# Performance work log

Hardware: AMD Instinct MI355X
Metric: run time of the kernel (lower is better)

The kernel has to match this reference:

```python
import jax, jax.numpy as jnp
import numpy as np

THRESH = 1.0
NBITS = 3
QMAX = float(2 ** NBITS - 1)
BN_EPS = 1e-5

T, B, IN_DIM = 500, 64, 440
HID, NLAYERS, OUT = 1024, 4, 1944


def fsq(v):
    # FakeSpikeQuantization (eval): quantize membrane potential to multiples of
    # threshold, clipped to [0, 2^n_bits - 1] levels; straight-through estimator.
    q = jnp.clip(jnp.round(v / THRESH), 0.0, QMAX) * THRESH
    return v + jax.lax.stop_gradient(q - v)


def input_fsq_scan(xs):
    # vmem += x; out = fsq(vmem); vmem -= out  -- sequential over time
    def step(vmem, x):
        vmem = vmem + x
        o = fsq(vmem)
        return vmem - o, o
    _, outs = jax.lax.scan(step, jnp.zeros_like(xs[0]), xs)
    return outs


def lif_scan(ws, tau):
    # syn = w_t + tau*prev_syn; vmem += syn; out = fsq(vmem); vmem -= out
    Bb, H = ws.shape[1], ws.shape[2]
    def step(carry, w_t):
        prev_syn, vmem = carry
        syn = w_t + tau * prev_syn
        vmem = vmem + syn
        o = fsq(vmem)
        return (syn, vmem - o), o
    init = (jnp.zeros((Bb, H), ws.dtype), jnp.zeros((Bb, H), ws.dtype))
    _, outs = jax.lax.scan(step, init, ws)
    return outs


def bn_eval(x, gamma, beta):
    # BatchNorm1d in eval mode with default running stats (mean=0, var=1)
    return x / jnp.sqrt(1.0 + BN_EPS) * gamma + beta


def setup_inputs() -> dict:
    key = jax.random.key(0)
    ks = jax.random.split(key, 10)
    xs = jax.random.normal(ks[0], (T, B, IN_DIM), dtype=jnp.float32)
    # kaiming-uniform-like init scales
    W0 = jax.random.uniform(ks[1], (HID, IN_DIM), minval=-1.0, maxval=1.0) * np.sqrt(1.0 / IN_DIM)
    Ws = jax.random.uniform(ks[2], (NLAYERS - 1, HID, HID), minval=-1.0, maxval=1.0) * np.sqrt(1.0 / HID)
    taus = jnp.ones((NLAYERS, HID), dtype=jnp.float32)
    bn_gamma = jnp.ones((NLAYERS, HID), dtype=jnp.float32)
    bn_beta = jnp.zeros((NLAYERS, HID), dtype=jnp.float32)
    bound = np.sqrt(0.01 / (HID + OUT))
    Wf = jax.random.uniform(ks[3], (OUT, HID), minval=-bound, maxval=bound).astype(jnp.float32)
    fbn_gamma = jnp.ones((OUT,), dtype=jnp.float32)
    fbn_beta = jnp.zeros((OUT,), dtype=jnp.float32)
    return {"xs": xs, "W0": W0, "Ws": Ws, "taus": taus, "bn_gamma": bn_gamma,
            "bn_beta": bn_beta, "Wf": Wf, "fbn_gamma": fbn_gamma, "fbn_beta": fbn_beta}


def reference(xs, W0, Ws, taus, bn_gamma, bn_beta, Wf, fbn_gamma, fbn_beta):
    # input spike quantization
    inps = input_fsq_scan(xs)  # [T,B,IN]
    n_layers = taus.shape[0]
    for l in range(n_layers):
        W = W0 if l == 0 else Ws[l - 1]
        ws = jnp.einsum('tbi,hi->tbh', inps, W)          # dense projection (no bias; use_bn)
        ws = bn_eval(ws, bn_gamma[l], bn_beta[l])
        inps = lif_scan(ws, taus[l])                     # [T,B,H]
    logits = jnp.einsum('tbh,oh->tbo', inps, Wf)         # final linear (no bias)
    logits = bn_eval(logits, fbn_gamma, fbn_beta)
    Tt, Bb, O = logits.shape
    return jax.nn.log_softmax(logits.reshape(Tt * Bb, O), axis=1)
```

## Files before the change

### kernel.cpp

```cpp
#include <hip/hip_runtime.h>
#include <hip/hip_bf16.h>
#include <cstddef>

typedef signed char i8;
typedef unsigned int u32;
typedef int intx4 __attribute__((ext_vector_type(4)));
typedef float floatx4 __attribute__((ext_vector_type(4)));

#define T_STEPS 500
#define BATCH 64
#define INDIM 440
#define INPAD 512
#define HID 1024
#define OUTDIM 1944
#define OUTPAD 2048
#define MROWS 32000
#define INV_SQRT_BN 0.9999950000374997f
#define CH 20

__device__ __forceinline__ void g2lds16(const void* g, void* l) {
  __builtin_amdgcn_global_load_lds(
      (const __attribute__((address_space(1))) u32*)g,
      (__attribute__((address_space(3))) u32*)l, 16, 0, 0);
}

__global__ __launch_bounds__(256) void input_fsq_k(const float* __restrict__ xs,
                                                   i8* __restrict__ sp0) {
  int tid = blockIdx.x * 256 + threadIdx.x;
  int b = tid >> 9;
  int i = tid & 511;
  bool act = (i < INDIM);
  const float* src = xs + (size_t)b * INDIM + (act ? i : (INDIM - 1));
  i8* dst = sp0 + (size_t)b * INPAD + i;
  float fact = act ? 1.f : 0.f;
  const int LS = BATCH * INDIM;
  const int SS = BATCH * INPAD;
  float vmem = 0.f;
  float bufA[CH], bufB[CH];
#pragma unroll
  for (int j = 0; j < CH; ++j) bufA[j] = src[(size_t)j * LS];
  for (int it = 0; it < 12; ++it) {
    const int t0 = it * 2 * CH;
#pragma unroll
    for (int j = 0; j < CH; ++j) bufB[j] = src[(size_t)(t0 + CH + j) * LS];
#pragma unroll
    for (int j = 0; j < CH; ++j) {
      vmem += bufA[j] * fact;
      float q = fminf(fmaxf(rintf(vmem), 0.f), 7.f);
      vmem -= q;
      dst[(size_t)(t0 + j) * SS] = (i8)q;
    }
#pragma unroll
    for (int j = 0; j < CH; ++j) bufA[j] = src[(size_t)(t0 + 2 * CH + j) * LS];
#pragma unroll
    for (int j = 0; j < CH; ++j) {
      vmem += bufB[j] * fact;
      float q = fminf(fmaxf(rintf(vmem), 0.f), 7.f);
      vmem -= q;
      dst[(size_t)(t0 + CH + j) * SS] = (i8)q;
    }
  }
  const int t0 = 24 * CH;
#pragma unroll
  for (int j = 0; j < CH; ++j) {
    vmem += bufA[j] * fact;
    float q = fminf(fmaxf(rintf(vmem), 0.f), 7.f);
    vmem -= q;
    dst[(size_t)(t0 + j) * SS] = (i8)q;
  }
}

__global__ __launch_bounds__(256) void lif_k(const float* __restrict__ ws,
                                             const float* __restrict__ taus,
                                             i8* __restrict__ sp) {
  int tid = blockIdx.x * 256 + threadIdx.x;
  float tau = taus[tid & (HID - 1)];
  const float* src = ws + tid;
  i8* dst = sp + tid;
  const int S = BATCH * HID;
  float syn = 0.f, vmem = 0.f;
  float bufA[CH], bufB[CH];
#pragma unroll
  for (int j = 0; j < CH; ++j) bufA[j] = src[(size_t)j * S];
  for (int it = 0; it < 12; ++it) {
    const int t0 = it * 2 * CH;
#pragma unroll
    for (int j = 0; j < CH; ++j) bufB[j] = src[(size_t)(t0 + CH + j) * S];
#pragma unroll
    for (int j = 0; j < CH; ++j) {
      syn = fmaf(tau, syn, bufA[j]);
      vmem += syn;
      float q = fminf(fmaxf(rintf(vmem), 0.f), 7.f);
      vmem -= q;
      dst[(size_t)(t0 + j) * S] = (i8)q;
    }
#pragma unroll
    for (int j = 0; j < CH; ++j) bufA[j] = src[(size_t)(t0 + 2 * CH + j) * S];
#pragma unroll
    for (int j = 0; j < CH; ++j) {
      syn = fmaf(tau, syn, bufB[j]);
      vmem += syn;
      float q = fminf(fmaxf(rintf(vmem), 0.f), 7.f);
      vmem -= q;
      dst[(size_t)(t0 + CH + j) * S] = (i8)q;
    }
  }
  const int t0 = 24 * CH;
#pragma unroll
  for (int j = 0; j < CH; ++j) {
    syn = fmaf(tau, syn, bufA[j]);
    vmem += syn;
    float q = fminf(fmaxf(rintf(vmem), 0.f), 7.f);
    vmem -= q;
    dst[(size_t)(t0 + j) * S] = (i8)q;
  }
}

__global__ __launch_bounds__(256) void quant_rows_k(
    const float* __restrict__ W, const float* __restrict__ g,
    i8* __restrict__ Q1, i8* __restrict__ Q2,
    float* __restrict__ S1, float* __restrict__ S2,
    int K_in, int K_out, int nvalid) {
  int row = blockIdx.x * 4 + (threadIdx.x >> 6);
  int lane = threadIdx.x & 63;
  bool valid = row < nvalid;
  float gm = valid ? g[row] * INV_SQRT_BN : 0.f;
  const float* src = W + (size_t)row * K_in;
  float w[16], r[16];
  const int ne = K_out >> 6;
  float mx = 0.f;
  for (int e = 0; e < ne; ++e) {
    int k = lane + (e << 6);
    float v = (valid && k < K_in) ? src[k] * gm : 0.f;
    w[e] = v;
    mx = fmaxf(mx, fabsf(v));
  }
#pragma unroll
  for (int o = 32; o; o >>= 1) mx = fmaxf(mx, __shfl_xor(mx, o));
  float s1 = (mx > 0.f) ? mx * (1.f / 127.f) : 1.f;
  float inv1 = 1.f / s1;
  float mr = 0.f;
  for (int e = 0; e < ne; ++e) {
    float q = fminf(fmaxf(rintf(w[e] * inv1), -127.f), 127.f);
    Q1[(size_t)row * K_out + lane + (e << 6)] = (i8)q;
    float res = fmaf(-s1, q, w[e]);
    r[e] = res;
    mr = fmaxf(mr, fabsf(res));
  }
#pragma unroll
  for (int o = 32; o; o >>= 1) mr = fmaxf(mr, __shfl_xor(mr, o));
  float s2 = (mr > 0.f) ? mr * (1.f / 127.f) : 1.f;
  float inv2 = 1.f / s2;
  for (int e = 0; e < ne; ++e) {
    float q = fminf(fmaxf(rintf(r[e] * inv2), -127.f), 127.f);
    Q2[(size_t)row * K_out + lane + (e << 6)] = (i8)q;
  }
  if (lane == 0) {
    S1[row] = s1;
    S2[row] = s2;
  }
}

template <int DUAL>
__global__ __launch_bounds__(256, 2) void gemm_i8(
    const i8* __restrict__ A, const i8* __restrict__ B1q,
    const i8* __restrict__ B2q, const float* __restrict__ S1,
    const float* __restrict__ S2, const float* __restrict__ bias,
    float* __restrict__ C, int K, int ldc, int ncols) {
  extern __shared__ char smem[];
  char* As = smem;
  char* Bs1 = As + 128 * 128;
  char* Bs2 = DUAL ? Bs1 + 128 * 128 : Bs1;

  const int tid = threadIdx.x;
  const int m0 = blockIdx.y * 128;
  const int n0 = blockIdx.x * 128;
  const int lane = tid & 63;
  const int wave = tid >> 6;
  const int wm = (wave & 1) * 64;
  const int wn = (wave >> 1) * 64;
  const int lr = lane & 15;
  const int lq = lane >> 4;

  intx4 acc1[4][4], acc2[DUAL ? 4 : 1][4];
#pragma unroll
  for (int i = 0; i < 4; ++i)
#pragma unroll
    for (int j = 0; j < 4; ++j) {
      intx4 z = {0, 0, 0, 0};
      acc1[i][j] = z;
      if (DUAL) acc2[i][j] = z;
    }

  const int srow = tid >> 3;
  const int sj = (tid & 7) ^ (srow & 7);
  const i8* ga = A + (size_t)(m0 + srow) * K + sj * 16;
  const i8* gb1 = B1q + (size_t)(n0 + srow) * K + sj * 16;
  const i8* gb2 = DUAL ? B2q + (size_t)(n0 + srow) * K + sj * 16 : (const i8*)nullptr;
  const int ldso = tid * 16;
  const int sw = lr & 7;

  for (int k0 = 0; k0 < K; k0 += 128) {
#pragma unroll
    for (int it = 0; it < 4; ++it) {
      g2lds16(ga + (size_t)(it * 32) * K + k0, As + ldso + it * 4096);
      g2lds16(gb1 + (size_t)(it * 32) * K + k0, Bs1 + ldso + it * 4096);
      if (DUAL) g2lds16(gb2 + (size_t)(it * 32) * K + k0, Bs2 + ldso + it * 4096);
    }
    __syncthreads();
#pragma unroll
    for (int kk = 0; kk < 2; ++kk) {
      const int jc = kk * 4 + lq;
      const int co = ((jc ^ sw) << 4);
      intx4 af[4];
#pragma unroll
      for (int i = 0; i < 4; ++i)
        af[i] = *(const intx4*)(As + (wm + i * 16 + lr) * 128 + co);
#pragma unroll
      for (int j = 0; j < 4; ++j) {
        const int bo = (wn + j * 16 + lr) * 128 + co;
        intx4 b1 = *(const intx4*)(Bs1 + bo);
#pragma unroll
        for (int i = 0; i < 4; ++i)
          acc1[i][j] = __builtin_amdgcn_mfma_i32_16x16x64_i8(af[i], b1, acc1[i][j], 0, 0, 0);
        if (DUAL) {
          intx4 b2 = *(const intx4*)(Bs2 + bo);
#pragma unroll
          for (int i = 0; i < 4; ++i)
            acc2[i][j] = __builtin_amdgcn_mfma_i32_16x16x64_i8(af[i], b2, acc2[i][j], 0, 0, 0);
        }
      }
    }
    __syncthreads();
  }

  float* Es = (float*)smem;
  const int rq = lq * 4;
  const int rbase = (wave & 1) * 16;
  float s1v[4], s2v[4], bv[4];
#pragma unroll
  for (int j = 0; j < 4; ++j) {
    int cg = n0 + wn + j * 16 + lr;
    s1v[j] = S1[cg];
    s2v[j] = DUAL ? S2[cg] : 0.f;
    bv[j] = (cg < ncols) ? bias[cg] : 0.f;
  }
#pragma unroll
  for (int i = 0; i < 4; ++i) {
    __syncthreads();
#pragma unroll
    for (int j = 0; j < 4; ++j) {
      int cl = wn + j * 16 + lr;
#pragma unroll
      for (int r = 0; r < 4; ++r) {
        float v = fmaf(s1v[j], (float)acc1[i][j][r], bv[j]);
        if (DUAL) v = fmaf(s2v[j], (float)acc2[i][j][r], v);
        Es[(rbase + rq + r) * 132 + cl] = v;
      }
    }
    __syncthreads();
#pragma unroll
    for (int ps = 0; ps < 4; ++ps) {
      int rl = ps * 8 + (tid >> 5);
      int c4 = (tid & 31) * 4;
      floatx4 v = *(const floatx4*)(Es + rl * 132 + c4);
      int rg = m0 + (rl >> 4) * 64 + i * 16 + (rl & 15);
      int cg = n0 + c4;
      if (cg < ncols)
        *(floatx4*)(C + (size_t)rg * ldc + cg) = v;
    }
  }
}

__global__ __launch_bounds__(256) void logsoftmax_k(float* __restrict__ data) {
  __shared__ float red[8];
  float* p = data + (size_t)blockIdx.x * OUTDIM;
  const int t = threadIdx.x;
  float v[8];
  float mx = -1e30f;
#pragma unroll
  for (int j = 0; j < 8; ++j) {
    int c = t + j * 256;
    v[j] = (c < OUTDIM) ? p[c] : -1e30f;
    mx = fmaxf(mx, v[j]);
  }
#pragma unroll
  for (int o = 32; o > 0; o >>= 1) mx = fmaxf(mx, __shfl_down(mx, o));
  if ((t & 63) == 0) red[t >> 6] = mx;
  __syncthreads();
  mx = fmaxf(fmaxf(red[0], red[1]), fmaxf(red[2], red[3]));
  float s = 0.f;
#pragma unroll
  for (int j = 0; j < 8; ++j) {
    int c = t + j * 256;
    if (c < OUTDIM) s += __expf(v[j] - mx);
  }
#pragma unroll
  for (int o = 32; o > 0; o >>= 1) s += __shfl_down(s, o);
  if ((t & 63) == 0) red[4 + (t >> 6)] = s;
  __syncthreads();
  s = (red[4] + red[5]) + (red[6] + red[7]);
  float lse = mx + __logf(s);
#pragma unroll
  for (int j = 0; j < 8; ++j) {
    int c = t + j * 256;
    if (c < OUTDIM) p[c] = v[j] - lse;
  }
}

extern "C" void kernel_launch(void* const* d_in, const int* in_sizes, int n_in,
                              void* d_out, int out_size, void* d_ws, size_t ws_size,
                              hipStream_t stream) {
  const float* xs = (const float*)d_in[0];
  const float* W0 = (const float*)d_in[1];
  const float* Ws = (const float*)d_in[2];
  const float* taus = (const float*)d_in[3];
  const float* bng = (const float*)d_in[4];
  const float* bnb = (const float*)d_in[5];
  const float* Wf = (const float*)d_in[6];
  const float* fg = (const float*)d_in[7];
  const float* fb = (const float*)d_in[8];
  float* out = (float*)d_out;

  char* p = (char*)d_ws;
  i8* sp0 = (i8*)p;    p += (size_t)MROWS * INPAD;
  i8* sp = (i8*)p;     p += (size_t)MROWS * HID;
  float* wsb = (float*)p; p += (size_t)MROWS * HID * 4;
  i8* Q1_0 = (i8*)p;   p += (size_t)HID * INPAD;
  i8* Q2_0 = (i8*)p;   p += (size_t)HID * INPAD;
  i8* Q1_l = (i8*)p;   p += (size_t)3 * HID * HID;
  i8* Q2_l = (i8*)p;   p += (size_t)3 * HID * HID;
  i8* Q1_f = (i8*)p;   p += (size_t)OUTPAD * HID;
  i8* Q2_f = (i8*)p;   p += (size_t)OUTPAD * HID;
  float* S1_0 = (float*)p; p += HID * 4;
  float* S2_0 = (float*)p; p += HID * 4;
  float* S1_l = (float*)p; p += 3 * HID * 4;
  float* S2_l = (float*)p; p += 3 * HID * 4;
  float* S1_f = (float*)p; p += OUTPAD * 4;
  float* S2_f = (float*)p; p += OUTPAD * 4;

  input_fsq_k<<<(BATCH * INPAD) / 256, 256, 0, stream>>>(xs, sp0);
  quant_rows_k<<<HID / 4, 256, 0, stream>>>(W0, bng, Q1_0, Q2_0, S1_0, S2_0,
                                            INDIM, INPAD, HID);
  for (int l = 1; l < 4; ++l)
    quant_rows_k<<<HID / 4, 256, 0, stream>>>(
        Ws + (size_t)(l - 1) * HID * HID, bng + l * HID,
        Q1_l + (size_t)(l - 1) * HID * HID, Q2_l + (size_t)(l - 1) * HID * HID,
        S1_l + (l - 1) * HID, S2_l + (l - 1) * HID, HID, HID, HID);
  quant_rows_k<<<OUTPAD / 4, 256, 0, stream>>>(Wf, fg, Q1_f, Q2_f, S1_f, S2_f,
                                               HID, HID, OUTDIM);

  gemm_i8<1><<<dim3(HID / 128, MROWS / 128), 256, 48 * 1024, stream>>>(
      sp0, Q1_0, Q2_0, S1_0, S2_0, bnb, wsb, INPAD, HID, HID);
  lif_k<<<(BATCH * HID) / 256, 256, 0, stream>>>(wsb, taus, sp);
  for (int l = 1; l < 4; ++l) {
    gemm_i8<1><<<dim3(HID / 128, MROWS / 128), 256, 48 * 1024, stream>>>(
        sp, Q1_l + (size_t)(l - 1) * HID * HID, Q2_l + (size_t)(l - 1) * HID * HID,
        S1_l + (l - 1) * HID, S2_l + (l - 1) * HID, bnb + l * HID, wsb,
        HID, HID, HID);
    lif_k<<<(BATCH * HID) / 256, 256, 0, stream>>>(wsb, taus + l * HID, sp);
  }
  gemm_i8<0><<<dim3(OUTPAD / 128, MROWS / 128), 256, 32 * 1024, stream>>>(
      sp, Q1_f, (const i8*)nullptr, S1_f, (const float*)nullptr, fb, out,
      HID, OUTDIM, OUTDIM);
  logsoftmax_k<<<MROWS, 256, 0, stream>>>(out);
}
```

Before: 893.4 us.

## Double-buffer A tile in LDS and stream B fragments directly from global

```diff
diff --git a/kernel.cpp b/kernel.cpp
--- a/kernel.cpp
+++ b/kernel.cpp
@@ -166,96 +166,136 @@
     const i8* __restrict__ A, const i8* __restrict__ B1q,
     const i8* __restrict__ B2q, const float* __restrict__ S1,
     const float* __restrict__ S2, const float* __restrict__ bias,
-    float* __restrict__ C, int K, int ldc, int ncols) {
+    float* __restrict__ C, int K, int NT, int ldc, int ncols) {
   extern __shared__ char smem[];
-  char* As = smem;
-  char* Bs1 = As + 128 * 128;
-  char* Bs2 = DUAL ? Bs1 + 128 * 128 : Bs1;
 
   const int tid = threadIdx.x;
   const int m0 = blockIdx.y * 128;
   const int n0 = blockIdx.x * 128;
   const int lane = tid & 63;
   const int wave = tid >> 6;
-  const int wm = (wave & 1) * 64;
-  const int wn = (wave >> 1) * 64;
   const int lr = lane & 15;
   const int lq = lane >> 4;
-
-  intx4 acc1[4][4], acc2[DUAL ? 4 : 1][4];
-#pragma unroll
-  for (int i = 0; i < 4; ++i)
-#pragma unroll
-    for (int j = 0; j < 4; ++j) {
+  const int wn = wave * 32;
+
+  const int srow = tid >> 3;
+  const int sj = (tid & 7) ^ (srow & 7);
+  const i8* gaP[4];
+#pragma unroll
+  for (int it = 0; it < 4; ++it)
+    gaP[it] = A + (size_t)(m0 + it * 32 + srow) * K + sj * 16;
+  const int ldso = tid * 16;
+
+  const i8* pb[2][2];
+#pragma unroll
+  for (int j = 0; j < 2; ++j) {
+    pb[0][j] = B1q + (size_t)(n0 + wn + j * 16 + lr) * K + lq * 16;
+    pb[1][j] = DUAL ? B2q + (size_t)(n0 + wn + j * 16 + lr) * K + lq * 16
+                    : pb[0][j];
+  }
+
+  intx4 acc1[8][2], acc2[DUAL ? 8 : 1][2];
+#pragma unroll
+  for (int i = 0; i < 8; ++i)
+#pragma unroll
+    for (int j = 0; j < 2; ++j) {
       intx4 z = {0, 0, 0, 0};
       acc1[i][j] = z;
       if (DUAL) acc2[i][j] = z;
     }
 
-  const int srow = tid >> 3;
-  const int sj = (tid & 7) ^ (srow & 7);
-  const i8* ga = A + (size_t)(m0 + srow) * K + sj * 16;
-  const i8* gb1 = B1q + (size_t)(n0 + srow) * K + sj * 16;
-  const i8* gb2 = DUAL ? B2q + (size_t)(n0 + srow) * K + sj * 16 : (const i8*)nullptr;
-  const int ldso = tid * 16;
   const int sw = lr & 7;
 
-  for (int k0 = 0; k0 < K; k0 += 128) {
-#pragma unroll
-    for (int it = 0; it < 4; ++it) {
-      g2lds16(ga + (size_t)(it * 32) * K + k0, As + ldso + it * 4096);
-      g2lds16(gb1 + (size_t)(it * 32) * K + k0, Bs1 + ldso + it * 4096);
-      if (DUAL) g2lds16(gb2 + (size_t)(it * 32) * K + k0, Bs2 + ldso + it * 4096);
-    }
-    __syncthreads();
+#pragma unroll
+  for (int it = 0; it < 4; ++it)
+    g2lds16(gaP[it], smem + ldso + it * 4096);
+
+  for (int t = 0; t < NT; ++t) {
+    const bool last = (t == NT - 1);
+    char* cur = smem + (t & 1) * 16384;
+    char* nxt = smem + ((t & 1) ^ 1) * 16384;
+
+    intx4 b1[2][2], b2[2][2];
+#pragma unroll
+    for (int kk = 0; kk < 2; ++kk)
+#pragma unroll
+      for (int j = 0; j < 2; ++j) {
+        b1[kk][j] = *(const intx4*)(pb[0][j] + kk * 64);
+        if (DUAL) b2[kk][j] = *(const intx4*)(pb[1][j] + kk * 64);
+      }
+    __builtin_amdgcn_sched_barrier(0);
+    if (!last) {
+#pragma unroll
+      for (int it = 0; it < 4; ++it) {
+        gaP[it] += 128;
+        g2lds16(gaP[it], nxt + ldso + it * 4096);
+      }
+    }
+    __builtin_amdgcn_sched_barrier(0);
+    if (!last) {
+      if (DUAL) asm volatile("s_waitcnt vmcnt(12)" ::: "memory");
+      else      asm volatile("s_waitcnt vmcnt(8)" ::: "memory");
+    } else {
+      if (DUAL) asm volatile("s_waitcnt vmcnt(8)" ::: "memory");
+      else      asm volatile("s_waitcnt vmcnt(4)" ::: "memory");
+    }
+    __builtin_amdgcn_sched_barrier(0);
+    __builtin_amdgcn_s_barrier();
+    __builtin_amdgcn_sched_barrier(0);
+
 #pragma unroll
     for (int kk = 0; kk < 2; ++kk) {
-      const int jc = kk * 4 + lq;
-      const int co = ((jc ^ sw) << 4);
-      intx4 af[4];
-#pragma unroll
-      for (int i = 0; i < 4; ++i)
-        af[i] = *(const intx4*)(As + (wm + i * 16 + lr) * 128 + co);
-#pragma unroll
-      for (int j = 0; j < 4; ++j) {
-        const int bo = (wn + j * 16 + lr) * 128 + co;
-        intx4 b1 = *(const intx4*)(Bs1 + bo);
-#pragma unroll
-        for (int i = 0; i < 4; ++i)
-          acc1[i][j] = __builtin_amdgcn_mfma_i32_16x16x64_i8(af[i], b1, acc1[i][j], 0, 0, 0);
+      intx4 af[8];
+#pragma unroll
+      for (int i = 0; i < 8; ++i)
+        af[i] = *(const intx4*)(cur + (i * 16 + lr) * 128 +
+                                (((kk * 4 + lq) ^ sw) << 4));
+#pragma unroll
+      for (int j = 0; j < 2; ++j) {
+#pragma unroll
+        for (int i = 0; i < 8; ++i)
+          acc1[i][j] = __builtin_amdgcn_mfma_i32_16x16x64_i8(
+              af[i], b1[kk][j], acc1[i][j], 0, 0, 0);
         if (DUAL) {
-          intx4 b2 = *(const intx4*)(Bs2 + bo);
-#pragma unroll
-          for (int i = 0; i < 4; ++i)
-            acc2[i][j] = __builtin_amdgcn_mfma_i32_16x16x64_i8(af[i], b2, acc2[i][j], 0, 0, 0);
+#pragma unroll
+          for (int i = 0; i < 8; ++i)
+            acc2[i][j] = __builtin_amdgcn_mfma_i32_16x16x64_i8(
+                af[i], b2[kk][j], acc2[i][j], 0, 0, 0);
         }
       }
     }
-    __syncthreads();
+    __builtin_amdgcn_s_barrier();
+#pragma unroll
+    for (int j = 0; j < 2; ++j) {
+      pb[0][j] += 128;
+      if (DUAL) pb[1][j] += 128;
+    }
   }
 
   float* Es = (float*)smem;
-  const int rq = lq * 4;
-  const int rbase = (wave & 1) * 16;
-  float s1v[4], s2v[4], bv[4];
-#pragma unroll
-  for (int j = 0; j < 4; ++j) {
+  float s1v[2], s2v[2], bv[2];
+#pragma unroll
+  for (int j = 0; j < 2; ++j) {
     int cg = n0 + wn + j * 16 + lr;
     s1v[j] = S1[cg];
     s2v[j] = DUAL ? S2[cg] : 0.f;
     bv[j] = (cg < ncols) ? bias[cg] : 0.f;
   }
 #pragma unroll
-  for (int i = 0; i < 4; ++i) {
+  for (int s = 0; s < 4; ++s) {
     __syncthreads();
 #pragma unroll
-    for (int j = 0; j < 4; ++j) {
-      int cl = wn + j * 16 + lr;
-#pragma unroll
-      for (int r = 0; r < 4; ++r) {
-        float v = fmaf(s1v[j], (float)acc1[i][j][r], bv[j]);
-        if (DUAL) v = fmaf(s2v[j], (float)acc2[i][j][r], v);
-        Es[(rbase + rq + r) * 132 + cl] = v;
+    for (int ii = 0; ii < 2; ++ii) {
+      int i = s * 2 + ii;
+#pragma unroll
+      for (int j = 0; j < 2; ++j) {
+        int cl = wn + j * 16 + lr;
+#pragma unroll
+        for (int r = 0; r < 4; ++r) {
+          float v = fmaf(s1v[j], (float)acc1[i][j][r], bv[j]);
+          if (DUAL) v = fmaf(s2v[j], (float)acc2[i][j][r], v);
+          Es[(ii * 16 + lq * 4 + r) * 132 + cl] = v;
+        }
       }
     }
     __syncthreads();
@@ -264,7 +304,7 @@
       int rl = ps * 8 + (tid >> 5);
       int c4 = (tid & 31) * 4;
       floatx4 v = *(const floatx4*)(Es + rl * 132 + c4);
-      int rg = m0 + (rl >> 4) * 64 + i * 16 + (rl & 15);
+      int rg = m0 + s * 32 + rl;
       int cg = n0 + c4;
       if (cg < ncols)
         *(floatx4*)(C + (size_t)rg * ldc + cg) = v;
@@ -350,18 +390,18 @@
   quant_rows_k<<<OUTPAD / 4, 256, 0, stream>>>(Wf, fg, Q1_f, Q2_f, S1_f, S2_f,
                                                HID, HID, OUTDIM);
 
-  gemm_i8<1><<<dim3(HID / 128, MROWS / 128), 256, 48 * 1024, stream>>>(
-      sp0, Q1_0, Q2_0, S1_0, S2_0, bnb, wsb, INPAD, HID, HID);
+  gemm_i8<1><<<dim3(HID / 128, MROWS / 128), 256, 32 * 1024, stream>>>(
+      sp0, Q1_0, Q2_0, S1_0, S2_0, bnb, wsb, INPAD, INPAD / 128, HID, HID);
   lif_k<<<(BATCH * HID) / 256, 256, 0, stream>>>(wsb, taus, sp);
   for (int l = 1; l < 4; ++l) {
-    gemm_i8<1><<<dim3(HID / 128, MROWS / 128), 256, 48 * 1024, stream>>>(
+    gemm_i8<1><<<dim3(HID / 128, MROWS / 128), 256, 32 * 1024, stream>>>(
         sp, Q1_l + (size_t)(l - 1) * HID * HID, Q2_l + (size_t)(l - 1) * HID * HID,
         S1_l + (l - 1) * HID, S2_l + (l - 1) * HID, bnb + l * HID, wsb,
-        HID, HID, HID);
+        HID, HID / 128, HID, HID);
     lif_k<<<(BATCH * HID) / 256, 256, 0, stream>>>(wsb, taus + l * HID, sp);
   }
   gemm_i8<0><<<dim3(OUTPAD / 128, MROWS / 128), 256, 32 * 1024, stream>>>(
       sp, Q1_f, (const i8*)nullptr, S1_f, (const float*)nullptr, fb, out,
-      HID, OUTDIM, OUTDIM);
+      HID, HID / 128, OUTDIM, OUTDIM);
   logsoftmax_k<<<MROWS, 256, 0, stream>>>(out);
 }
```

Result: slower. 959.3 us (+7.4%).
